# Performance work log

Hardware: AMD Instinct MI355X
Metric: run time of the kernel (lower is better)

## Reference

```python
import jax, jax.numpy as jnp
import numpy as np

NUM_USER = 50000
NUM_ITEM = 30000
N_NODES = NUM_USER + NUM_ITEM
N_EDGES = 1_000_000
FEAT_DIM = 768
DIM_LATENT = 128
DIM_ID = 64
NEG_SLOPE = 0.01  # F.leaky_relu default


def leaky_relu(x):
    return jnp.where(x >= 0, x, NEG_SLOPE * x)


def l2_normalize(x, eps=1e-12):
    # F.normalize(dim=-1): divide by clamped L2 norm
    n = jnp.sqrt(jnp.sum(x * x, axis=-1, keepdims=True))
    return x / jnp.maximum(n, eps)


def graph_gat(x, W, edge_index, num_nodes):
    """MGAT GraphGAT: x -> x@W, gated inner-product attention, softmax over
    incoming edges per destination node, scatter-add, L2 normalize."""
    x = x @ W                                    # [N, D]
    src = edge_index[0]                          # j (source)
    dst = edge_index[1]                          # i (target)
    x_j = x[src]                                 # [E, D]
    x_i = x[dst]                                 # [E, D]
    inner = jnp.sum(x_i * x_j, axis=-1)          # [E]
    # gate: sigmoid(deg(src)^-0.5 * inner)
    deg = jax.ops.segment_sum(jnp.ones_like(inner), src, num_segments=num_nodes)
    gate = jax.nn.sigmoid(deg[src] ** -0.5 * inner)
    score = inner * gate                         # [E]
    # segment softmax over destination nodes
    smax = jax.ops.segment_max(score, dst, num_segments=num_nodes)
    e = jnp.exp(score - smax[dst])
    denom = jax.ops.segment_sum(e, dst, num_segments=num_nodes)
    alpha = e / (denom[dst] + 1e-16)             # [E]
    out = jax.ops.segment_sum(x_j * alpha[:, None], dst, num_segments=num_nodes)
    return l2_normalize(out)


def setup_inputs() -> dict:
    key = jax.random.key(0)
    ks = jax.random.split(key, 16)

    def xavier(k, shape):
        fan_in, fan_out = shape[0], shape[1]
        std = float(np.sqrt(2.0 / (fan_in + fan_out)))
        return jax.random.normal(k, shape, dtype=jnp.float32) * std

    features = jax.random.normal(ks[0], (NUM_ITEM, FEAT_DIM), dtype=jnp.float32)
    id_embedding = jax.random.normal(ks[1], (N_NODES, DIM_ID), dtype=jnp.float32)
    # edge_index [2, E] with no self-loops (remove_self_loops is then identity)
    src = jax.random.randint(ks[2], (N_EDGES,), 0, N_NODES)
    off = jax.random.randint(ks[3], (N_EDGES,), 1, N_NODES)
    dst = (src + off) % N_NODES
    edge_index = jnp.stack([src, dst]).astype(jnp.int64)

    return {
        "features": features,
        "id_embedding": id_embedding,
        "edge_index": edge_index,
        "preference": xavier(ks[4], (NUM_USER, DIM_LATENT)),
        "mlp_w": xavier(ks[5], (FEAT_DIM, DIM_LATENT)),
        "mlp_b": jnp.zeros((DIM_LATENT,), dtype=jnp.float32),
        "conv1_w": xavier(ks[6], (DIM_LATENT, DIM_LATENT)),
        "lin1_w": xavier(ks[7], (DIM_LATENT, DIM_ID)),
        "lin1_b": jnp.zeros((DIM_ID,), dtype=jnp.float32),
        "g1_w": xavier(ks[8], (DIM_LATENT, DIM_ID)),
        "g1_b": jnp.zeros((DIM_ID,), dtype=jnp.float32),
        "conv2_w": xavier(ks[9], (DIM_ID, DIM_ID)),
        "lin2_w": xavier(ks[10], (DIM_ID, DIM_ID)),
        "lin2_b": jnp.zeros((DIM_ID,), dtype=jnp.float32),
        "g2_w": xavier(ks[11], (DIM_ID, DIM_ID)),
        "g2_b": jnp.zeros((DIM_ID,), dtype=jnp.float32),
    }


def reference(features, id_embedding, edge_index, preference, mlp_w, mlp_b,
              conv1_w, lin1_w, lin1_b, g1_w, g1_b,
              conv2_w, lin2_w, lin2_b, g2_w, g2_b):
    temp_features = jnp.tanh(features @ mlp_w + mlp_b)        # [num_item, dim_latent]
    x = jnp.concatenate([preference, temp_features], axis=0)  # [N, dim_latent]
    x = l2_normalize(x)

    h = leaky_relu(graph_gat(x, conv1_w, edge_index, N_NODES))
    x_hat = leaky_relu(x @ lin1_w + lin1_b) + id_embedding
    x1 = leaky_relu(h @ g1_w + g1_b + x_hat)                  # [N, dim_id]

    h = leaky_relu(graph_gat(x1, conv2_w, edge_index, N_NODES))
    x_hat = leaky_relu(x1 @ lin2_w + lin2_b) + id_embedding
    x2 = leaky_relu(h @ g2_w + g2_b + x_hat)                  # [N, dim_id]

    return jnp.concatenate([x1, x2], axis=1)                  # [N, 2*dim_id]
```

## Files before the change

kernel.cpp:

```cpp
#include <hip/hip_runtime.h>
#include <hip/hip_bf16.h>
#include <math.h>

#define NUM_USER 50000
#define NUM_ITEM 30000
#define N_NODES  80000
#define N_EDGES  1000000
#define FEAT_DIM 768
#define DLAT 128
#define DID  64
#define NEG_SLOPE 0.01f
#define CAP 64

#define NB_COUNT ((N_EDGES + 255) / 256)
#define NB_WT 560
#define NB_MLP ((NUM_ITEM + 63) / 64)
#define NB_NORM (N_NODES / 8)
#define NB_RSQ ((N_NODES + 511) / 512)
#define NB_CONV1 (N_NODES / 64)

__device__ __forceinline__ float leaky(float v) { return v >= 0.f ? v : NEG_SLOPE * v; }

__device__ __forceinline__ float wave_reduce_sum(float v) {
#pragma unroll
    for (int off = 32; off > 0; off >>= 1) v += __shfl_xor(v, off, 64);
    return v;
}

__device__ __forceinline__ unsigned short f2bf(float f) {
    unsigned int u = __float_as_uint(f);
    unsigned int r = u + 0x7fffu + ((u >> 16) & 1u);
    return (unsigned short)(r >> 16);
}
__device__ __forceinline__ float bf2f(unsigned short h) {
    return __uint_as_float(((unsigned int)h) << 16);
}

typedef __attribute__((ext_vector_type(8))) short short8v;
typedef __attribute__((ext_vector_type(4))) float f32x4;

__device__ __forceinline__ void unpack8(int4 v, float* f) {
    unsigned int u;
    u = (unsigned int)v.x; f[0] = __uint_as_float(u << 16); f[1] = __uint_as_float(u & 0xFFFF0000u);
    u = (unsigned int)v.y; f[2] = __uint_as_float(u << 16); f[3] = __uint_as_float(u & 0xFFFF0000u);
    u = (unsigned int)v.z; f[4] = __uint_as_float(u << 16); f[5] = __uint_as_float(u & 0xFFFF0000u);
    u = (unsigned int)v.w; f[6] = __uint_as_float(u << 16); f[7] = __uint_as_float(u & 0xFFFF0000u);
}

__device__ __forceinline__ void split_store8(
    float4 a, float4 b, unsigned short* dh, unsigned short* dl)
{
    float v[8] = {a.x, a.y, a.z, a.w, b.x, b.y, b.z, b.w};
    unsigned int ph[4], pl[4];
#pragma unroll
    for (int i = 0; i < 4; i++) {
        unsigned short h0 = f2bf(v[2*i]),   l0 = f2bf(v[2*i]   - bf2f(h0));
        unsigned short h1 = f2bf(v[2*i+1]), l1 = f2bf(v[2*i+1] - bf2f(h1));
        ph[i] = (unsigned int)h0 | ((unsigned int)h1 << 16);
        pl[i] = (unsigned int)l0 | ((unsigned int)l1 << 16);
    }
    *(int4*)dh = make_int4((int)ph[0], (int)ph[1], (int)ph[2], (int)ph[3]);
    *(int4*)dl = make_int4((int)pl[0], (int)pl[1], (int)pl[2], (int)pl[3]);
}


__device__ __forceinline__ void prep_one(int id, const float* W, int KK, int NN,
                                         unsigned short* Wh, unsigned short* Wl)
{
    int n = id / KK, k = id - n * KK;
    float v = W[(size_t)k * NN + n];
    unsigned short h = f2bf(v);
    Wh[id] = h;
    Wl[id] = f2bf(v - bf2f(h));
}

__device__ void wt_prep_body(int pb,
    const float* mlp_w, const float* c1, const float* l1, const float* g1,
    const float* c2, const float* l2, const float* g2,
    unsigned short* mlpWh, unsigned short* mlpWl,
    unsigned short* wc1h, unsigned short* wc1l,
    unsigned short* wl1h, unsigned short* wl1l,
    unsigned short* wg1h, unsigned short* wg1l,
    unsigned short* wc2h, unsigned short* wc2l,
    unsigned short* wl2h, unsigned short* wl2l,
    unsigned short* wg2h, unsigned short* wg2l)
{
    int id = pb * 256 + threadIdx.x;
    if (id < 98304)       prep_one(id,          mlp_w, FEAT_DIM, DLAT, mlpWh, mlpWl);
    else if (id < 114688) prep_one(id - 98304,  c1, DLAT, DLAT, wc1h, wc1l);
    else if (id < 122880) prep_one(id - 114688, l1, DLAT, DID,  wl1h, wl1l);
    else if (id < 131072) prep_one(id - 122880, g1, DLAT, DID,  wg1h, wg1l);
    else if (id < 135168) prep_one(id - 131072, c2, DID,  DID,  wc2h, wc2l);
    else if (id < 139264) prep_one(id - 135168, l2, DID,  DID,  wl2h, wl2l);
    else if (id < 143360) prep_one(id - 139264, g2, DID,  DID,  wg2h, wg2l);
}

__device__ void fill_body(int pb, const int* src, const int* dst,
                          int* deg_out, int* cursor, int* csr_pad)
{
    int e = pb * 256 + threadIdx.x;
    if (e < N_EDGES) {
        int s = src[e], d = dst[e];
        atomicAdd(&deg_out[s], 1);
        int slot = atomicAdd(&cursor[d], 1);
        if (slot < CAP) csr_pad[(size_t)d * CAP + slot] = s;
    }
}

__device__ void mlp_body(int pb, const float* F,
    const unsigned short* Wh, const unsigned short* Wl,
    const float* bias, float* xout)
{
    __shared__ unsigned short sAh[64][72];
    __shared__ unsigned short sAl[64][72];
    __shared__ unsigned short sWh[128][72];
    __shared__ unsigned short sWlo[128][72];

    const int tid = threadIdx.x;
    const int lane = tid & 63;
    const int w = tid >> 6;
    const int wr = w >> 1, wc = w & 1;
    const int r0 = pb * 64;

    f32x4 acc[2][4];
#pragma unroll
    for (int m = 0; m < 2; m++)
#pragma unroll
        for (int n = 0; n < 4; n++) acc[m][n] = (f32x4){0.f, 0.f, 0.f, 0.f};

    for (int kc = 0; kc < FEAT_DIM; kc += 64) {
#pragma unroll
        for (int it = 0; it < 2; it++) {
            int slot = tid + it * 256;
            int row = slot >> 3;
            int k8 = (slot & 7) * 8;
            int gr = r0 + row;
            float4 a = make_float4(0.f, 0.f, 0.f, 0.f), b = a;
            if (gr < NUM_ITEM) {
                const float4* p = (const float4*)(F + (size_t)gr * FEAT_DIM + kc + k8);
                a = p[0]; b = p[1];
            }
            split_store8(a, b, &sAh[row][k8], &sAl[row][k8]);
        }
#pragma unroll
        for (int it = 0; it < 4; it++) {
            int slot = tid + it * 256;
            int n = slot >> 3;
            int k8 = (slot & 7) * 8;
            *(int4*)&sWh[n][k8]  = *(const int4*)(Wh + (size_t)n * FEAT_DIM + kc + k8);
            *(int4*)&sWlo[n][k8] = *(const int4*)(Wl + (size_t)n * FEAT_DIM + kc + k8);
        }
        __syncthreads();

#pragma unroll
        for (int k0 = 0; k0 < 64; k0 += 32) {
            int klane = k0 + (lane >> 4) * 8;
            short8v ah[2], al[2], bh[4], bl[4];
#pragma unroll
            for (int m = 0; m < 2; m++) {
                int row = wr * 32 + m * 16 + (lane & 15);
                ah[m] = *(const short8v*)&sAh[row][klane];
                al[m] = *(const short8v*)&sAl[row][klane];
            }
#pragma unroll
            for (int n = 0; n < 4; n++) {
                int col = wc * 64 + n * 16 + (lane & 15);
                bh[n] = *(const short8v*)&sWh[col][klane];
                bl[n] = *(const short8v*)&sWlo[col][klane];
            }
#pragma unroll
            for (int m = 0; m < 2; m++)
#pragma unroll
                for (int n = 0; n < 4; n++) {
                    acc[m][n] = __builtin_amdgcn_mfma_f32_16x16x32_bf16(ah[m], bh[n], acc[m][n], 0, 0, 0);
                    acc[m][n] = __builtin_amdgcn_mfma_f32_16x16x32_bf16(ah[m], bl[n], acc[m][n], 0, 0, 0);
                    acc[m][n] = __builtin_amdgcn_mfma_f32_16x16x32_bf16(al[m], bh[n], acc[m][n], 0, 0, 0);
                }
        }
        __syncthreads();
    }

#pragma unroll
    for (int m = 0; m < 2; m++) {
        int rbase = r0 + wr * 32 + m * 16 + (lane >> 4) * 4;
#pragma unroll
        for (int n = 0; n < 4; n++) {
            int col = wc * 64 + n * 16 + (lane & 15);
            float bv = bias[col];
#pragma unroll
            for (int q = 0; q < 4; q++) {
                int gr = rbase + q;
                if (gr < NUM_ITEM)
                    xout[(size_t)gr * DLAT + col] = tanhf(acc[m][n][q] + bv);
            }
        }
    }
}

__device__ void normcopy_body(int pb, const float* pref, float* x)
{
    int wid = pb * 8 + (threadIdx.x >> 6);
    if (wid >= N_NODES) return;
    int lane = threadIdx.x & 63;
    const float* srow = (wid < NUM_USER) ? (pref + (size_t)wid * DLAT)
                                         : (x + (size_t)wid * DLAT);
    float v0 = srow[lane], v1 = srow[lane + 64];
    float s = wave_reduce_sum(v0 * v0 + v1 * v1);
    float inv = 1.0f / fmaxf(sqrtf(s), 1e-12f);
    float* drow = x + (size_t)wid * DLAT;
    drow[lane] = v0 * inv;
    drow[lane + 64] = v1 * inv;
}

template<int K, int NC>
__device__ void conv_body(int pb, const float* X, int ldx,
    const unsigned short* Wth, const unsigned short* Wtl,
    unsigned short* O, int ldo)
{
    constexpr int NW = NC / 64;
    constexpr int MW = 4 / NW;
    constexpr int WROWS = 64 / MW;
    constexpr int MF = WROWS / 16;
    constexpr int KSTEPS = K / 32;
    constexpr int KP = K + 8;

    __shared__ unsigned short sAh[64][KP];
    __shared__ unsigned short sAl[64][KP];

    const int tid = threadIdx.x;
    const int lane = tid & 63;
    const int w = tid >> 6;
    const int wr = w / NW, wc = w % NW;
    const int r0 = pb * 64;

#pragma unroll
    for (int it = 0; it < K / 32; it++) {
        int slot = tid + it * 256;
        int row = slot / (K / 8);
        int k8 = (slot % (K / 8)) * 8;
        const float4* p = (const float4*)(X + (size_t)(r0 + row) * ldx + k8);
        split_store8(p[0], p[1], &sAh[row][k8], &sAl[row][k8]);
    }
    __syncthreads();

    f32x4 acc[MF][4];
#pragma unroll
    for (int m = 0; m < MF; m++)
#pragma unroll
        for (int n = 0; n < 4; n++) acc[m][n] = (f32x4){0.f, 0.f, 0.f, 0.f};

#pragma unroll
    for (int ks = 0; ks < KSTEPS; ks++) {
        int klane = ks * 32 + (lane >> 4) * 8;
        short8v ah[MF], al[MF];
#pragma unroll
        for (int m = 0; m < MF; m++) {
            int row = wr * WROWS + m * 16 + (lane & 15);
            ah[m] = *(const short8v*)&sAh[row][klane];
            al[m] = *(const short8v*)&sAl[row][klane];
        }
#pragma unroll
        for (int n = 0; n < 4; n++) {
            int col = wc * 64 + n * 16 + (lane & 15);
            short8v bh = *(const short8v*)(Wth + (size_t)col * K + klane);
            short8v bl = *(const short8v*)(Wtl + (size_t)col * K + klane);
#pragma unroll
            for (int m = 0; m < MF; m++) {
                acc[m][n] = __builtin_amdgcn_mfma_f32_16x16x32_bf16(ah[m], bh, acc[m][n], 0, 0, 0);
                acc[m][n] = __builtin_amdgcn_mfma_f32_16x16x32_bf16(ah[m], bl, acc[m][n], 0, 0, 0);
                acc[m][n] = __builtin_amdgcn_mfma_f32_16x16x32_bf16(al[m], bh, acc[m][n], 0, 0, 0);
            }
        }
    }

#pragma unroll
    for (int m = 0; m < MF; m++) {
        int rbase = r0 + wr * WROWS + m * 16 + (lane >> 4) * 4;
#pragma unroll
        for (int n = 0; n < 4; n++) {
            int col = wc * 64 + n * 16 + (lane & 15);
#pragma unroll
            for (int q = 0; q < 4; q++)
                O[(size_t)(rbase + q) * ldo + col] = f2bf(acc[m][n][q]);
        }
    }
}


__global__ __launch_bounds__(256) void k_fill_wtprep(
    const int* __restrict__ src, const int* __restrict__ dst,
    int* __restrict__ deg_out, int* __restrict__ cursor, int* __restrict__ csr_pad,
    const float* __restrict__ mlp_w, const float* __restrict__ c1,
    const float* __restrict__ l1, const float* __restrict__ g1,
    const float* __restrict__ c2, const float* __restrict__ l2,
    const float* __restrict__ g2,
    unsigned short* __restrict__ mlpWh, unsigned short* __restrict__ mlpWl,
    unsigned short* __restrict__ wc1h, unsigned short* __restrict__ wc1l,
    unsigned short* __restrict__ wl1h, unsigned short* __restrict__ wl1l,
    unsigned short* __restrict__ wg1h, unsigned short* __restrict__ wg1l,
    unsigned short* __restrict__ wc2h, unsigned short* __restrict__ wc2l,
    unsigned short* __restrict__ wl2h, unsigned short* __restrict__ wl2l,
    unsigned short* __restrict__ wg2h, unsigned short* __restrict__ wg2l)
{
    int b = blockIdx.x;
    if (b < NB_COUNT) fill_body(b, src, dst, deg_out, cursor, csr_pad);
    else wt_prep_body(b - NB_COUNT, mlp_w, c1, l1, g1, c2, l2, g2,
                      mlpWh, mlpWl, wc1h, wc1l, wl1h, wl1l, wg1h, wg1l,
                      wc2h, wc2l, wl2h, wl2l, wg2h, wg2l);
}

__global__ __launch_bounds__(256) void mlp_kernel(
    const float* __restrict__ F, const unsigned short* __restrict__ Wh,
    const unsigned short* __restrict__ Wl, const float* __restrict__ bias,
    float* __restrict__ xout)
{
    mlp_body(blockIdx.x, F, Wh, Wl, bias, xout);
}

__global__ __launch_bounds__(512) void k_norm_rsq(
    const float* __restrict__ pref, float* __restrict__ x,
    const int* __restrict__ deg_out, float* __restrict__ rsq)
{
    int b = blockIdx.x;
    if (b < NB_NORM) normcopy_body(b, pref, x);
    else {
        int gid = (b - NB_NORM) * 512 + threadIdx.x;
        if (gid < N_NODES) rsq[gid] = rsqrtf((float)deg_out[gid]);
    }
}

__global__ __launch_bounds__(256) void conv1_kernel(
    const float* __restrict__ X,
    const unsigned short* __restrict__ Wth, const unsigned short* __restrict__ Wtl,
    unsigned short* __restrict__ O)
{
    conv_body<DLAT, DLAT>(blockIdx.x, X, DLAT, Wth, Wtl, O, DLAT);
}

__global__ __launch_bounds__(256) void conv2_kernel(
    const float* __restrict__ X, int ldx,
    const unsigned short* __restrict__ Wth, const unsigned short* __restrict__ Wtl,
    unsigned short* __restrict__ O, int ldo)
{
    conv_body<DID, DID>(blockIdx.x, X, ldx, Wth, Wtl, O, ldo);
}

template<int D>
__global__ __launch_bounds__(256) void gat_layer_kernel(
    const unsigned short* __restrict__ xw, const int* __restrict__ cnt,
    const int* __restrict__ csr_pad, const float* __restrict__ rsq_deg,
    float* __restrict__ h)
{
    constexpr int SG  = D / 8;
    constexpr int EPC = 64 / SG;
    int wid = blockIdx.x * 4 + (threadIdx.x >> 6);
    if (wid >= N_NODES) return;
    const int lane = threadIdx.x & 63;
    const int g = lane / SG;
    const int t = lane % SG;
    const int n_e = min(cnt[wid], CAP);
    const int* bucket = csr_pad + (size_t)wid * CAP;

    float xd[8];
    unpack8(*(const int4*)(xw + (size_t)wid * D + 8 * t), xd);

    float l = 0.f;
    float acc[8];
#pragma unroll
    for (int c = 0; c < 8; c++) acc[c] = 0.f;

    for (int base = 0; base < n_e; base += EPC) {
        int i = base + g;
        bool valid = (i < n_e);
        int s = valid ? bucket[i] : 0;
        float a[8];
        unpack8(*(const int4*)(xw + (size_t)s * D + 8 * t), a);
        float p = a[0]*xd[0] + a[1]*xd[1] + a[2]*xd[2] + a[3]*xd[3]
                + a[4]*xd[4] + a[5]*xd[5] + a[6]*xd[6] + a[7]*xd[7];
#pragma unroll
        for (int off = SG / 2; off > 0; off >>= 1) p += __shfl_xor(p, off, 64);
        float rsd = valid ? rsq_deg[s] : 1.f;
        float gate = 1.0f / (1.0f + __expf(-(p * rsd)));
        float sc = fminf(p * gate, 80.f);
        float w = valid ? __expf(sc) : 0.f;
        l += w;
#pragma unroll
        for (int c = 0; c < 8; c++) acc[c] += w * a[c];
    }

#pragma unroll
    for (int off = SG; off < 64; off <<= 1) {
        l += __shfl_xor(l, off, 64);
#pragma unroll
        for (int c = 0; c < 8; c++) acc[c] += __shfl_xor(acc[c], off, 64);
    }

    float invl = 1.0f / (l + 1e-16f);
    float ss = 0.f;
#pragma unroll
    for (int c = 0; c < 8; c++) { acc[c] *= invl; ss += acc[c] * acc[c]; }
#pragma unroll
    for (int off = SG / 2; off > 0; off >>= 1) ss += __shfl_xor(ss, off, 64);
    float inv = 1.0f / fmaxf(sqrtf(ss), 1e-12f);

    if (g == 0) {
        float4 o0, o1;
        o0.x = leaky(acc[0] * inv); o0.y = leaky(acc[1] * inv);
        o0.z = leaky(acc[2] * inv); o0.w = leaky(acc[3] * inv);
        o1.x = leaky(acc[4] * inv); o1.y = leaky(acc[5] * inv);
        o1.z = leaky(acc[6] * inv); o1.w = leaky(acc[7] * inv);
        float* op = h + (size_t)wid * D + 8 * t;
        *(float4*)(op) = o0;
        *(float4*)(op + 4) = o1;
    }
}

template<int K>
__global__ __launch_bounds__(256) void combine_mfma_kernel(
    const float* __restrict__ H, int ldh,
    const float* __restrict__ X, int ldx,
    const unsigned short* __restrict__ Gth, const unsigned short* __restrict__ Gtl,
    const unsigned short* __restrict__ Lth, const unsigned short* __restrict__ Ltl,
    const float* __restrict__ g_b, const float* __restrict__ lin_b,
    const float* __restrict__ id_emb, float* __restrict__ out, int out_off)
{
    constexpr int KSTEPS = K / 32;
    constexpr int KP = K + 8;

    __shared__ unsigned short sHh[64][KP];
    __shared__ unsigned short sHl[64][KP];
    __shared__ unsigned short sXh[64][KP];
    __shared__ unsigned short sXl[64][KP];

    const int tid = threadIdx.x;
    const int lane = tid & 63;
    const int wr = tid >> 6;
    const int r0 = blockIdx.x * 64;

#pragma unroll
    for (int it = 0; it < K / 32; it++) {
        int slot = tid + it * 256;
        int row = slot / (K / 8);
        int k8 = (slot % (K / 8)) * 8;
        const float4* ph = (const float4*)(H + (size_t)(r0 + row) * ldh + k8);
        split_store8(ph[0], ph[1], &sHh[row][k8], &sHl[row][k8]);
        const float4* px = (const float4*)(X + (size_t)(r0 + row) * ldx + k8);
        split_store8(px[0], px[1], &sXh[row][k8], &sXl[row][k8]);
    }
    __syncthreads();

    f32x4 accG[4], accL[4];
#pragma unroll
    for (int n = 0; n < 4; n++) {
        accG[n] = (f32x4){0.f, 0.f, 0.f, 0.f};
        accL[n] = (f32x4){0.f, 0.f, 0.f, 0.f};
    }

#pragma unroll
    for (int ks = 0; ks < KSTEPS; ks++) {
        int klane = ks * 32 + (lane >> 4) * 8;
        int row = wr * 16 + (lane & 15);
        short8v hh = *(const short8v*)&sHh[row][klane];
        short8v hl = *(const short8v*)&sHl[row][klane];
        short8v xh = *(const short8v*)&sXh[row][klane];
        short8v xl = *(const short8v*)&sXl[row][klane];
#pragma unroll
        for (int n = 0; n < 4; n++) {
            int col = n * 16 + (lane & 15);
            short8v gh = *(const short8v*)(Gth + (size_t)col * K + klane);
            short8v gl = *(const short8v*)(Gtl + (size_t)col * K + klane);
            short8v lh = *(const short8v*)(Lth + (size_t)col * K + klane);
            short8v ll = *(const short8v*)(Ltl + (size_t)col * K + klane);
            accG[n] = __builtin_amdgcn_mfma_f32_16x16x32_bf16(hh, gh, accG[n], 0, 0, 0);
            accG[n] = __builtin_amdgcn_mfma_f32_16x16x32_bf16(hh, gl, accG[n], 0, 0, 0);
            accG[n] = __builtin_amdgcn_mfma_f32_16x16x32_bf16(hl, gh, accG[n], 0, 0, 0);
            accL[n] = __builtin_amdgcn_mfma_f32_16x16x32_bf16(xh, lh, accL[n], 0, 0, 0);
            accL[n] = __builtin_amdgcn_mfma_f32_16x16x32_bf16(xh, ll, accL[n], 0, 0, 0);
            accL[n] = __builtin_amdgcn_mfma_f32_16x16x32_bf16(xl, lh, accL[n], 0, 0, 0);
        }
    }

    int rbase = r0 + wr * 16 + (lane >> 4) * 4;
#pragma unroll
    for (int n = 0; n < 4; n++) {
        int col = n * 16 + (lane & 15);
        float gb = g_b[col], lb = lin_b[col];
#pragma unroll
        for (int q = 0; q < 4; q++) {
            int gr = rbase + q;
            float xhv = leaky(accL[n][q] + lb) + id_emb[(size_t)gr * DID + col];
            float v = leaky(accG[n][q] + gb + xhv);
            out[(size_t)gr * (2 * DID) + out_off + col] = v;
        }
    }
}

extern "C" void kernel_launch(void* const* d_in, const int* in_sizes, int n_in,
                              void* d_out, int out_size, void* d_ws, size_t ws_size,
                              hipStream_t stream)
{
    const float* features = (const float*)d_in[0];
    const float* id_emb   = (const float*)d_in[1];
    const int*   ei       = (const int*)d_in[2];
    const float* pref     = (const float*)d_in[3];
    const float* mlp_w    = (const float*)d_in[4];
    const float* mlp_b    = (const float*)d_in[5];
    const float* conv1_w  = (const float*)d_in[6];
    const float* lin1_w   = (const float*)d_in[7];
    const float* lin1_b   = (const float*)d_in[8];
    const float* g1_w     = (const float*)d_in[9];
    const float* g1_b     = (const float*)d_in[10];
    const float* conv2_w  = (const float*)d_in[11];
    const float* lin2_w   = (const float*)d_in[12];
    const float* lin2_b   = (const float*)d_in[13];
    const float* g2_w     = (const float*)d_in[14];
    const float* g2_b     = (const float*)d_in[15];
    const int* src = ei;
    const int* dst = ei + N_EDGES;
    float* out = (float*)d_out;

    float* x        = (float*)d_ws;
    unsigned short* xwb = (unsigned short*)(x + (size_t)N_NODES * DLAT);
    float* gat      = (float*)(xwb + (size_t)N_NODES * DLAT);
    int*   deg_out  = (int*)(gat + (size_t)N_NODES * DLAT);
    int*   cnt      = deg_out + N_NODES;
    int*   csr_pad  = cnt + N_NODES;
    float* rsq_deg  = (float*)(csr_pad + (size_t)N_NODES * CAP);
    unsigned short* mlpWh = (unsigned short*)gat;
    unsigned short* mlpWl = mlpWh + (size_t)FEAT_DIM * DLAT;
    unsigned short* wbase = (unsigned short*)(
        (((uintptr_t)(rsq_deg + N_NODES)) + 15) & ~(uintptr_t)15);
    unsigned short* wc1h = wbase;
    unsigned short* wc1l = wc1h + 16384;
    unsigned short* wl1h = wc1l + 16384;
    unsigned short* wl1l = wl1h + 8192;
    unsigned short* wg1h = wl1l + 8192;
    unsigned short* wg1l = wg1h + 8192;
    unsigned short* wc2h = wg1l + 8192;
    unsigned short* wc2l = wc2h + 4096;
    unsigned short* wl2h = wc2l + 4096;
    unsigned short* wl2l = wl2h + 4096;
    unsigned short* wg2h = wl2l + 4096;
    unsigned short* wg2l = wg2h + 4096;

    hipMemsetAsync(deg_out, 0, 2 * N_NODES * sizeof(int), stream);

    k_fill_wtprep<<<NB_COUNT + NB_WT, 256, 0, stream>>>(
        src, dst, deg_out, cnt, csr_pad,
        mlp_w, conv1_w, lin1_w, g1_w, conv2_w, lin2_w, g2_w,
        mlpWh, mlpWl, wc1h, wc1l, wl1h, wl1l, wg1h, wg1l,
        wc2h, wc2l, wl2h, wl2l, wg2h, wg2l);

    mlp_kernel<<<NB_MLP, 256, 0, stream>>>(
        features, mlpWh, mlpWl, mlp_b, x + (size_t)NUM_USER * DLAT);

    k_norm_rsq<<<NB_NORM + NB_RSQ, 512, 0, stream>>>(pref, x, deg_out, rsq_deg);

    conv1_kernel<<<NB_CONV1, 256, 0, stream>>>(x, wc1h, wc1l, xwb);

    gat_layer_kernel<DLAT><<<(N_NODES + 3) / 4, 256, 0, stream>>>(
        xwb, cnt, csr_pad, rsq_deg, gat);
    combine_mfma_kernel<DLAT><<<N_NODES / 64, 256, 0, stream>>>(
        gat, DLAT, x, DLAT, wg1h, wg1l, wl1h, wl1l, g1_b, lin1_b, id_emb, out, 0);

    conv2_kernel<<<N_NODES / 64, 256, 0, stream>>>(out, 2 * DID, wc2h, wc2l, xwb, DID);
    gat_layer_kernel<DID><<<(N_NODES + 3) / 4, 256, 0, stream>>>(
        xwb, cnt, csr_pad, rsq_deg, gat);
    combine_mfma_kernel<DID><<<N_NODES / 64, 256, 0, stream>>>(
        gat, DID, out, 2 * DID, wg2h, wg2l, wl2h, wl2l, g2_b, lin2_b, id_emb, out, DID);
}
```

Before: 421.0 us.

## Fuse MLP GEMM into edge-fill kernel without LDS, splitting weights on the fly

Removes the separate MLP kernel and the mlp weight pre-split pass, and runs the feature MLP inside the edge-fill/weight-prep launch. Blocks are interleaved 6 fill to 1 MLP/prep so atomic-bound fill work overlaps compute. The new MLP body reads features and fp32 weights directly into registers and does the bf16 hi/lo split per block, dropping LDS and barriers. In exchange, weight loads are strided and uncoalesced, and every block repeats the weight conversion.

```diff
diff --git a/kernel.cpp b/kernel.cpp
--- a/kernel.cpp
+++ b/kernel.cpp
@@ -12,9 +12,10 @@
 #define NEG_SLOPE 0.01f
 #define CAP 64
 
-#define NB_COUNT ((N_EDGES + 255) / 256)
-#define NB_WT 560
-#define NB_MLP ((NUM_ITEM + 63) / 64)
+#define NB_FILL ((N_EDGES + 255) / 256)
+#define NB_MLPN ((NUM_ITEM + 63) / 64)
+#define NB_WT2 176
+#define NB_OTH (NB_MLPN + NB_WT2)
 #define NB_NORM (N_NODES / 8)
 #define NB_RSQ ((N_NODES + 511) / 512)
 #define NB_CONV1 (N_NODES / 64)
@@ -63,6 +64,19 @@
     *(int4*)dl = make_int4((int)pl[0], (int)pl[1], (int)pl[2], (int)pl[3]);
 }
 
+__device__ __forceinline__ void split8_reg(const float* v, short8v& h, short8v& l)
+{
+    union { short8v s; unsigned int u[4]; } H, L;
+#pragma unroll
+    for (int i = 0; i < 4; i++) {
+        unsigned short h0 = f2bf(v[2*i]),   l0 = f2bf(v[2*i]   - bf2f(h0));
+        unsigned short h1 = f2bf(v[2*i+1]), l1 = f2bf(v[2*i+1] - bf2f(h1));
+        H.u[i] = (unsigned int)h0 | ((unsigned int)h1 << 16);
+        L.u[i] = (unsigned int)l0 | ((unsigned int)l1 << 16);
+    }
+    h = H.s; l = L.s;
+}
+
 
 __device__ __forceinline__ void prep_one(int id, const float* W, int KK, int NN,
                                          unsigned short* Wh, unsigned short* Wl)
@@ -75,9 +89,8 @@
 }
 
 __device__ void wt_prep_body(int pb,
-    const float* mlp_w, const float* c1, const float* l1, const float* g1,
+    const float* c1, const float* l1, const float* g1,
     const float* c2, const float* l2, const float* g2,
-    unsigned short* mlpWh, unsigned short* mlpWl,
     unsigned short* wc1h, unsigned short* wc1l,
     unsigned short* wl1h, unsigned short* wl1l,
     unsigned short* wg1h, unsigned short* wg1l,
@@ -86,13 +99,12 @@
     unsigned short* wg2h, unsigned short* wg2l)
 {
     int id = pb * 256 + threadIdx.x;
-    if (id < 98304)       prep_one(id,          mlp_w, FEAT_DIM, DLAT, mlpWh, mlpWl);
-    else if (id < 114688) prep_one(id - 98304,  c1, DLAT, DLAT, wc1h, wc1l);
-    else if (id < 122880) prep_one(id - 114688, l1, DLAT, DID,  wl1h, wl1l);
-    else if (id < 131072) prep_one(id - 122880, g1, DLAT, DID,  wg1h, wg1l);
-    else if (id < 135168) prep_one(id - 131072, c2, DID,  DID,  wc2h, wc2l);
-    else if (id < 139264) prep_one(id - 135168, l2, DID,  DID,  wl2h, wl2l);
-    else if (id < 143360) prep_one(id - 139264, g2, DID,  DID,  wg2h, wg2l);
+    if (id < 16384)      prep_one(id,          c1, DLAT, DLAT, wc1h, wc1l);
+    else if (id < 24576) prep_one(id - 16384,  l1, DLAT, DID,  wl1h, wl1l);
+    else if (id < 32768) prep_one(id - 24576,  g1, DLAT, DID,  wg1h, wg1l);
+    else if (id < 36864) prep_one(id - 32768,  c2, DID,  DID,  wc2h, wc2l);
+    else if (id < 40960) prep_one(id - 36864,  l2, DID,  DID,  wl2h, wl2l);
+    else if (id < 45056) prep_one(id - 40960,  g2, DID,  DID,  wg2h, wg2l);
 }
 
 __device__ void fill_body(int pb, const int* src, const int* dst,
@@ -107,15 +119,9 @@
     }
 }
 
-__device__ void mlp_body(int pb, const float* F,
-    const unsigned short* Wh, const unsigned short* Wl,
-    const float* bias, float* xout)
-{
-    __shared__ unsigned short sAh[64][72];
-    __shared__ unsigned short sAl[64][72];
-    __shared__ unsigned short sWh[128][72];
-    __shared__ unsigned short sWlo[128][72];
-
+__device__ void mlp_nolds_body(int pb, const float* F, const float* W,
+                               const float* bias, float* xout)
+{
     const int tid = threadIdx.x;
     const int lane = tid & 63;
     const int w = tid >> 6;
@@ -128,56 +134,43 @@
 #pragma unroll
         for (int n = 0; n < 4; n++) acc[m][n] = (f32x4){0.f, 0.f, 0.f, 0.f};
 
-    for (int kc = 0; kc < FEAT_DIM; kc += 64) {
-#pragma unroll
-        for (int it = 0; it < 2; it++) {
-            int slot = tid + it * 256;
-            int row = slot >> 3;
-            int k8 = (slot & 7) * 8;
-            int gr = r0 + row;
-            float4 a = make_float4(0.f, 0.f, 0.f, 0.f), b = a;
-            if (gr < NUM_ITEM) {
-                const float4* p = (const float4*)(F + (size_t)gr * FEAT_DIM + kc + k8);
-                a = p[0]; b = p[1];
+    int rowm[2]; bool rowok[2];
+#pragma unroll
+    for (int m = 0; m < 2; m++) {
+        rowm[m] = r0 + wr * 32 + m * 16 + (lane & 15);
+        rowok[m] = rowm[m] < NUM_ITEM;
+    }
+
+    for (int ks = 0; ks < FEAT_DIM / 32; ks++) {
+        int k0 = ks * 32 + (lane >> 4) * 8;
+        short8v ah[2], al[2];
+#pragma unroll
+        for (int m = 0; m < 2; m++) {
+            float v[8] = {0.f, 0.f, 0.f, 0.f, 0.f, 0.f, 0.f, 0.f};
+            if (rowok[m]) {
+                const float4* p = (const float4*)(F + (size_t)rowm[m] * FEAT_DIM + k0);
+                float4 a = p[0], b = p[1];
+                v[0]=a.x; v[1]=a.y; v[2]=a.z; v[3]=a.w;
+                v[4]=b.x; v[5]=b.y; v[6]=b.z; v[7]=b.w;
             }
-            split_store8(a, b, &sAh[row][k8], &sAl[row][k8]);
-        }
-#pragma unroll
-        for (int it = 0; it < 4; it++) {
-            int slot = tid + it * 256;
-            int n = slot >> 3;
-            int k8 = (slot & 7) * 8;
-            *(int4*)&sWh[n][k8]  = *(const int4*)(Wh + (size_t)n * FEAT_DIM + kc + k8);
-            *(int4*)&sWlo[n][k8] = *(const int4*)(Wl + (size_t)n * FEAT_DIM + kc + k8);
-        }
-        __syncthreads();
-
-#pragma unroll
-        for (int k0 = 0; k0 < 64; k0 += 32) {
-            int klane = k0 + (lane >> 4) * 8;
-            short8v ah[2], al[2], bh[4], bl[4];
+            split8_reg(v, ah[m], al[m]);
+        }
+#pragma unroll
+        for (int n = 0; n < 4; n++) {
+            int col = wc * 64 + n * 16 + (lane & 15);
+            float vb[8];
+#pragma unroll
+            for (int j = 0; j < 8; j++)
+                vb[j] = W[(size_t)(k0 + j) * DLAT + col];
+            short8v bh, bl;
+            split8_reg(vb, bh, bl);
 #pragma unroll
             for (int m = 0; m < 2; m++) {
-                int row = wr * 32 + m * 16 + (lane & 15);
-                ah[m] = *(const short8v*)&sAh[row][klane];
-                al[m] = *(const short8v*)&sAl[row][klane];
+                acc[m][n] = __builtin_amdgcn_mfma_f32_16x16x32_bf16(ah[m], bh, acc[m][n], 0, 0, 0);
+                acc[m][n] = __builtin_amdgcn_mfma_f32_16x16x32_bf16(ah[m], bl, acc[m][n], 0, 0, 0);
+                acc[m][n] = __builtin_amdgcn_mfma_f32_16x16x32_bf16(al[m], bh, acc[m][n], 0, 0, 0);
             }
-#pragma unroll
-            for (int n = 0; n < 4; n++) {
-                int col = wc * 64 + n * 16 + (lane & 15);
-                bh[n] = *(const short8v*)&sWh[col][klane];
-                bl[n] = *(const short8v*)&sWlo[col][klane];
-            }
-#pragma unroll
-            for (int m = 0; m < 2; m++)
-#pragma unroll
-                for (int n = 0; n < 4; n++) {
-                    acc[m][n] = __builtin_amdgcn_mfma_f32_16x16x32_bf16(ah[m], bh[n], acc[m][n], 0, 0, 0);
-                    acc[m][n] = __builtin_amdgcn_mfma_f32_16x16x32_bf16(ah[m], bl[n], acc[m][n], 0, 0, 0);
-                    acc[m][n] = __builtin_amdgcn_mfma_f32_16x16x32_bf16(al[m], bh[n], acc[m][n], 0, 0, 0);
-                }
-        }
-        __syncthreads();
+        }
     }
 
 #pragma unroll
@@ -287,14 +280,14 @@
 }
 
 
-__global__ __launch_bounds__(256) void k_fill_wtprep(
+__global__ __launch_bounds__(256) void k_fill_mlp_wtprep(
     const int* __restrict__ src, const int* __restrict__ dst,
     int* __restrict__ deg_out, int* __restrict__ cursor, int* __restrict__ csr_pad,
-    const float* __restrict__ mlp_w, const float* __restrict__ c1,
-    const float* __restrict__ l1, const float* __restrict__ g1,
-    const float* __restrict__ c2, const float* __restrict__ l2,
-    const float* __restrict__ g2,
-    unsigned short* __restrict__ mlpWh, unsigned short* __restrict__ mlpWl,
+    const float* __restrict__ F, const float* __restrict__ mlp_w,
+    const float* __restrict__ mlp_b, float* __restrict__ xout,
+    const float* __restrict__ c1, const float* __restrict__ l1,
+    const float* __restrict__ g1, const float* __restrict__ c2,
+    const float* __restrict__ l2, const float* __restrict__ g2,
     unsigned short* __restrict__ wc1h, unsigned short* __restrict__ wc1l,
     unsigned short* __restrict__ wl1h, unsigned short* __restrict__ wl1l,
     unsigned short* __restrict__ wg1h, unsigned short* __restrict__ wg1l,
@@ -303,18 +296,21 @@
     unsigned short* __restrict__ wg2h, unsigned short* __restrict__ wg2l)
 {
     int b = blockIdx.x;
-    if (b < NB_COUNT) fill_body(b, src, dst, deg_out, cursor, csr_pad);
-    else wt_prep_body(b - NB_COUNT, mlp_w, c1, l1, g1, c2, l2, g2,
-                      mlpWh, mlpWl, wc1h, wc1l, wl1h, wl1l, wg1h, wg1l,
-                      wc2h, wc2l, wl2h, wl2l, wg2h, wg2l);
-}
-
-__global__ __launch_bounds__(256) void mlp_kernel(
-    const float* __restrict__ F, const unsigned short* __restrict__ Wh,
-    const unsigned short* __restrict__ Wl, const float* __restrict__ bias,
-    float* __restrict__ xout)
-{
-    mlp_body(blockIdx.x, F, Wh, Wl, bias, xout);
+    if (b < NB_OTH * 7) {
+        int grp = b / 7, rem = b - grp * 7;
+        if (rem < 6) {
+            int fb = grp * 6 + rem;
+            if (fb < NB_FILL) fill_body(fb, src, dst, deg_out, cursor, csr_pad);
+        } else {
+            if (grp < NB_MLPN) mlp_nolds_body(grp, F, mlp_w, mlp_b, xout);
+            else wt_prep_body(grp - NB_MLPN, c1, l1, g1, c2, l2, g2,
+                              wc1h, wc1l, wl1h, wl1l, wg1h, wg1l,
+                              wc2h, wc2l, wl2h, wl2l, wg2h, wg2l);
+        }
+    } else {
+        int fb = NB_OTH * 6 + (b - NB_OTH * 7);
+        if (fb < NB_FILL) fill_body(fb, src, dst, deg_out, cursor, csr_pad);
+    }
 }
 
 __global__ __launch_bounds__(512) void k_norm_rsq(
@@ -526,8 +522,6 @@
     int*   cnt      = deg_out + N_NODES;
     int*   csr_pad  = cnt + N_NODES;
     float* rsq_deg  = (float*)(csr_pad + (size_t)N_NODES * CAP);
-    unsigned short* mlpWh = (unsigned short*)gat;
-    unsigned short* mlpWl = mlpWh + (size_t)FEAT_DIM * DLAT;
     unsigned short* wbase = (unsigned short*)(
         (((uintptr_t)(rsq_deg + N_NODES)) + 15) & ~(uintptr_t)15);
     unsigned short* wc1h = wbase;
@@ -545,14 +539,12 @@
 
     hipMemsetAsync(deg_out, 0, 2 * N_NODES * sizeof(int), stream);
 
-    k_fill_wtprep<<<NB_COUNT + NB_WT, 256, 0, stream>>>(
+    k_fill_mlp_wtprep<<<NB_OTH * 7 + (NB_FILL - NB_OTH * 6), 256, 0, stream>>>(
         src, dst, deg_out, cnt, csr_pad,
-        mlp_w, conv1_w, lin1_w, g1_w, conv2_w, lin2_w, g2_w,
-        mlpWh, mlpWl, wc1h, wc1l, wl1h, wl1l, wg1h, wg1l,
+        features, mlp_w, mlp_b, x + (size_t)NUM_USER * DLAT,
+        conv1_w, lin1_w, g1_w, conv2_w, lin2_w, g2_w,
+        wc1h, wc1l, wl1h, wl1l, wg1h, wg1l,
         wc2h, wc2l, wl2h, wl2l, wg2h, wg2l);
-
-    mlp_kernel<<<NB_MLP, 256, 0, stream>>>(
-        features, mlpWh, mlpWl, mlp_b, x + (size_t)NUM_USER * DLAT);
 
     k_norm_rsq<<<NB_NORM + NB_RSQ, 512, 0, stream>>>(pref, x, deg_out, rsq_deg);
 
```

Measured after the change: 484.1 us. 15.0% more time.
